# Kernel tuning notes

Measured on AMD Instinct MI355X. Metric: run time of the kernel, lower is better.

Reference implementation:

```python
import math
import jax, jax.numpy as jnp
import numpy as np

B, SX, SY, D, H = 2, 1024, 1024, 1024, 16
FULL = 1536   # padded (full_q == full_k) frame length for the two-source attention
N_CTX = 2048  # causal bias buffer size
HD = D // H
LENS_X = np.array([1024, 700])
LENS_Y = np.array([1024, 850])


def _heads(t):
    b, s, d = t.shape
    return t.reshape(b, s, H, HD).transpose(0, 2, 1, 3)  # [B,H,S,HD]


def _merge(t):
    b, h, s, hd = t.shape
    return t.transpose(0, 2, 1, 3).reshape(b, s, h * hd)


def setup_inputs() -> dict:
    key = jax.random.key(0)
    ks = jax.random.split(key, 8)
    s = 0.02
    # ragged pack/unpack index lists: take = positions in the FULL frame, fill = positions in the shrunk frame
    x_take_b = np.concatenate([np.full(l, b, np.int32) for b, l in enumerate(LENS_X)])
    x_take_p = np.concatenate([(FULL - l + np.arange(l)).astype(np.int32) for l in LENS_X])  # right-aligned
    x_fill_b = x_take_b.copy()
    x_fill_p = np.concatenate([np.arange(l, dtype=np.int32) for l in LENS_X])
    y_take_b = np.concatenate([np.full(l, b, np.int32) for b, l in enumerate(LENS_Y)])
    y_take_p = np.concatenate([np.arange(l, dtype=np.int32) for l in LENS_Y])  # left-aligned
    y_fill_b = y_take_b.copy()
    y_fill_p = y_take_p.copy()
    # additive padding mask for the self-attention over shrunk x
    mask = np.full((B, 1, 1, SX), -10000.0, np.float32)
    for b, l in enumerate(LENS_X):
        mask[b, :, :, :l] = 0.0
    return {
        "x": jax.random.normal(ks[0], (B, SX, D), jnp.float32),
        "y": jax.random.normal(ks[1], (B, SY, D), jnp.float32),
        "attention_mask_x": jnp.asarray(mask),
        "W_attn": jax.random.normal(ks[2], (D, 3 * D), jnp.float32) * s,
        "b_attn": jnp.zeros((3 * D,), jnp.float32),
        "W_2a": jax.random.normal(ks[3], (D, D), jnp.float32) * s,
        "b_2a": jnp.zeros((D,), jnp.float32),
        "W_2b": jax.random.normal(ks[4], (D, 2 * D), jnp.float32) * s,
        "b_2b": jnp.zeros((2 * D,), jnp.float32),
        "W_proj": jax.random.normal(ks[5], (2 * D, D), jnp.float32) * s,
        "b_proj": jnp.zeros((D,), jnp.float32),
        "x_take_b": jnp.asarray(x_take_b), "x_take_p": jnp.asarray(x_take_p),
        "x_fill_b": jnp.asarray(x_fill_b), "x_fill_p": jnp.asarray(x_fill_p),
        "y_take_b": jnp.asarray(y_take_b), "y_take_p": jnp.asarray(y_take_p),
        "y_fill_b": jnp.asarray(y_fill_b), "y_fill_p": jnp.asarray(y_fill_p),
    }


def reference(x, y, attention_mask_x, W_attn, b_attn, W_2a, b_2a, W_2b, b_2b,
              W_proj, b_proj, x_take_b, x_take_p, x_fill_b, x_fill_p,
              y_take_b, y_take_p, y_fill_b, y_fill_p):
    causal = jnp.tril(jnp.ones((N_CTX, N_CTX), jnp.float32))
    inv_sqrt = 1.0 / math.sqrt(HD)

    # --- branch 1: causal self-attention on shrunk x ---
    qkv = x @ W_attn + b_attn
    q, k, v = jnp.split(qkv, 3, axis=2)
    q, k, v = _heads(q), _heads(k), _heads(v)
    w = jnp.einsum('bhqd,bhkd->bhqk', q, k) * inv_sqrt  # [B,H,SX,SX]
    b1 = causal[:SX, :SX]
    w = w * b1 - 10000.0 * (1.0 - b1) + attention_mask_x
    a = jnp.einsum('bhqk,bhkd->bhqd', jax.nn.softmax(w, axis=-1), v)
    a = _merge(a)  # [B,SX,D]

    # --- branch 2: two-source attention with ragged expand/shrink ---
    q2 = _heads(x @ W_2a + b_2a)                      # [B,H,SX,HD]
    k2, v2 = jnp.split(y @ W_2b + b_2b, 2, axis=2)
    k2, v2 = _heads(k2), _heads(v2)                   # [B,H,SY,HD]
    w2 = jnp.einsum('bhqd,bhkd->bhqk', q2, k2)        # [B,H,SX,SY] (unscaled yet)
    # expand key dim: shrunk SY -> FULL
    temp = jnp.zeros((B, H, SX, FULL), w2.dtype)
    temp = temp.at[y_take_b, :, :, y_take_p].set(w2[y_fill_b, :, :, y_fill_p])
    # expand query dim: shrunk SX -> FULL
    new_w = jnp.zeros((B, H, FULL, FULL), w2.dtype)
    new_w = new_w.at[x_take_b, :, x_take_p, :].set(temp[x_fill_b, :, x_fill_p, :])
    new_v = jnp.zeros((B, H, FULL, HD), v2.dtype)
    new_v = new_v.at[y_take_b, :, y_take_p, :].set(v2[y_fill_b, :, y_fill_p, :])
    kmask = jnp.full((B, 1, 1, FULL), -10000.0, w2.dtype)
    kmask = kmask.at[y_take_b, :, :, y_take_p].set(0.0)
    new_w = new_w * inv_sqrt
    b2 = causal[:FULL, :FULL]  # ns-nd == 0 since full_q == full_k
    new_w = new_w * b2 - 10000.0 * (1.0 - b2) + kmask
    a2 = jnp.einsum('bhqk,bhkd->bhqd', jax.nn.softmax(new_w, axis=-1), new_v)  # [B,H,FULL,HD]
    # shrink query dim back: FULL -> SX
    a2s = jnp.zeros((B, H, SX, HD), a2.dtype)
    a2s = a2s.at[x_fill_b, :, x_fill_p, :].set(a2[x_take_b, :, x_take_p, :])
    a2m = _merge(a2s)  # [B,SX,D]

    out = jnp.concatenate([a, a2m], axis=2) @ W_proj + b_proj  # [B,SX,D]
    return out
```

## Files before the change

kernel.cpp:

```cpp
#include <hip/hip_runtime.h>
#include <hip/hip_bf16.h>

typedef __bf16 bf16;
typedef __attribute__((ext_vector_type(4))) __bf16 bf16x4;
typedef __attribute__((ext_vector_type(8))) __bf16 bf16x8;
typedef __attribute__((ext_vector_type(4))) float floatx4;

__device__ __forceinline__ void gl_lds16(const bf16* g, bf16* l) {
  __builtin_amdgcn_global_load_lds(
      (const __attribute__((address_space(1))) void*)g,
      (__attribute__((address_space(3))) void*)l, 16, 0, 0);
}

__global__ __launch_bounds__(256) void sentinel_kernel(float* out, int n, float code) {
  int i = blockIdx.x * 256 + threadIdx.x;
  if (i < n) out[i] = code;
}

struct TP { const float* W; bf16* WT; int K; int N; int bxn; int bid0; };

__global__ __launch_bounds__(256) void prep_kernel(TP t0, TP t1, TP t2, TP t3,
                                                   const float* __restrict__ x,
                                                   const float* __restrict__ y,
                                                   bf16* __restrict__ xb,
                                                   bf16* __restrict__ yb) {
  __shared__ bf16 tile[32][33];
  int bid = blockIdx.x;
  if (bid < 8192) {
    TP t = t0;
    if (bid >= t3.bid0) t = t3;
    else if (bid >= t2.bid0) t = t2;
    else if (bid >= t1.bid0) t = t1;
    int rb = bid - t.bid0;
    int bx = rb % t.bxn, by = rb / t.bxn;
    int n0 = bx * 32, k0 = by * 32;
    int tx = threadIdx.x & 31, ty = threadIdx.x >> 5;
#pragma unroll
    for (int i = 0; i < 32; i += 8)
      tile[ty + i][tx] = (bf16)t.W[(size_t)(k0 + ty + i) * t.N + n0 + tx];
    __syncthreads();
#pragma unroll
    for (int i = 0; i < 32; i += 8)
      t.WT[(size_t)(n0 + ty + i) * t.K + k0 + tx] = tile[tx][ty + i];
  } else {
    long base = (long)(bid - 8192) * 4096 + (long)threadIdx.x * 16;
    const float* src = x; bf16* dst = xb; long idx = base;
    if (base >= 2097152) { src = y; dst = yb; idx = base - 2097152; }
    floatx4 v0 = *(const floatx4*)(src + idx);
    floatx4 v1 = *(const floatx4*)(src + idx + 4);
    floatx4 v2 = *(const floatx4*)(src + idx + 8);
    floatx4 v3 = *(const floatx4*)(src + idx + 12);
    bf16x8 o0, o1;
#pragma unroll
    for (int i = 0; i < 4; ++i) {
      o0[i] = (bf16)v0[i]; o0[4 + i] = (bf16)v1[i];
      o1[i] = (bf16)v2[i]; o1[4 + i] = (bf16)v3[i];
    }
    *(bf16x8*)(dst + idx) = o0;
    *(bf16x8*)(dst + idx + 8) = o1;
  }
}

struct GP { const bf16* A; const bf16* WT; const float* bias; bf16* C; bf16* VT;
            int N; int ldc; int vcol0; int bxn; int bid0; };

__global__ __launch_bounds__(256) void proj3_kernel(GP g0, GP g1, GP g2) {
  __shared__ __attribute__((aligned(16))) bf16 As[128 * 32];
  __shared__ __attribute__((aligned(16))) bf16 Bs[128 * 32];
  int bid = blockIdx.x;
  GP g = g0;
  if (bid >= g2.bid0) g = g2;
  else if (bid >= g1.bid0) g = g1;
  int rb = bid - g.bid0;
  int row0 = (rb / g.bxn) * 128, col0 = (rb % g.bxn) * 128;
  const int K = 1024;
  int tid = threadIdx.x;
  int lane = tid & 63, wave = tid >> 6;
  int quad = lane >> 4, l16 = lane & 15;
  int wm = wave >> 1, wn = wave & 1;
  floatx4 acc[4][4] = {};
  for (int k0 = 0; k0 < K; k0 += 32) {
#pragma unroll
    for (int s = 0; s < 2; ++s) {
      int chunk = s * 256 + tid;
      int r = chunk >> 2, c = (chunk & 3) * 8;
      gl_lds16(g.WT + (size_t)(col0 + r) * K + k0 + c, Bs + (size_t)chunk * 8);
      gl_lds16(g.A + (size_t)(row0 + r) * K + k0 + c, As + (size_t)chunk * 8);
    }
    __syncthreads();
    bf16x8 afr[4], bfr[4];
#pragma unroll
    for (int r = 0; r < 4; ++r)
      afr[r] = *(const bf16x8*)(As + (wm * 64 + r * 16 + l16) * 32 + quad * 8);
#pragma unroll
    for (int c = 0; c < 4; ++c)
      bfr[c] = *(const bf16x8*)(Bs + (wn * 64 + c * 16 + l16) * 32 + quad * 8);
#pragma unroll
    for (int r = 0; r < 4; ++r)
#pragma unroll
      for (int c = 0; c < 4; ++c)
        acc[r][c] = __builtin_amdgcn_mfma_f32_16x16x32_bf16(afr[r], bfr[c], acc[r][c], 0, 0, 0);
    __syncthreads();
  }
  int inV = (col0 >= g.vcol0);
#pragma unroll
  for (int c = 0; c < 4; ++c) {
    int gcol = col0 + wn * 64 + c * 16 + l16;
    float bv = g.bias[gcol];
    if (inV) {
      int vcol = gcol - g.vcol0;
      int hh = vcol >> 6, dd = vcol & 63;
#pragma unroll
      for (int r = 0; r < 4; ++r) {
        int row = row0 + wm * 64 + r * 16 + quad * 4;
        int bb = row >> 10, key = row & 1023;
        bf16x4 pk;
#pragma unroll
        for (int e = 0; e < 4; ++e) pk[e] = (bf16)(acc[r][c][e] + bv);
        *(bf16x4*)(g.VT + ((size_t)((bb << 4) + hh)) * 65536 + (size_t)dd * 1024 + key) = pk;
      }
    } else {
#pragma unroll
      for (int r = 0; r < 4; ++r) {
        int grow = row0 + wm * 64 + r * 16 + quad * 4;
#pragma unroll
        for (int e = 0; e < 4; ++e)
          g.C[(size_t)(grow + e) * g.ldc + gcol] = (bf16)(acc[r][c][e] + bv);
      }
    }
  }
}

__global__ __launch_bounds__(256) void gemm_out_kernel(const bf16* __restrict__ A,
                                                       const bf16* __restrict__ WT,
                                                       const float* __restrict__ bias,
                                                       float* __restrict__ C,
                                                       int N, int K) {
  __shared__ __attribute__((aligned(16))) bf16 As[64 * 32];
  __shared__ __attribute__((aligned(16))) bf16 Bs[64 * 32];
  int tid = threadIdx.x;
  int lane = tid & 63, wave = tid >> 6;
  int quad = lane >> 4, l16 = lane & 15;
  int row0 = blockIdx.y * 64, col0 = blockIdx.x * 64;
  floatx4 acc[4] = {};
  for (int k0 = 0; k0 < K; k0 += 32) {
    int r = tid >> 2, c = (tid & 3) * 8;
    gl_lds16(A + (size_t)(row0 + r) * K + k0 + c, As + (size_t)tid * 8);
    gl_lds16(WT + (size_t)(col0 + r) * K + k0 + c, Bs + (size_t)tid * 8);
    __syncthreads();
    bf16x8 af = *(const bf16x8*)(As + (wave * 16 + l16) * 32 + quad * 8);
#pragma unroll
    for (int nt = 0; nt < 4; ++nt) {
      bf16x8 bf = *(const bf16x8*)(Bs + (nt * 16 + l16) * 32 + quad * 8);
      acc[nt] = __builtin_amdgcn_mfma_f32_16x16x32_bf16(af, bf, acc[nt], 0, 0, 0);
    }
    __syncthreads();
  }
#pragma unroll
  for (int nt = 0; nt < 4; ++nt) {
    int gcol = col0 + nt * 16 + l16;
    float bv = bias[gcol];
#pragma unroll
    for (int e = 0; e < 4; ++e) {
      int grow = row0 + wave * 16 + quad * 4 + e;
      C[(size_t)grow * N + gcol] = acc[nt][e] + bv;
    }
  }
}

struct AP {
  const bf16* Q; const bf16* K; const bf16* VT; bf16* O;
  int qstride, kstride, ostride;
  long qbatch, kbatch, obatch;
  int coff0, coff1, klen0, klen1, qv0, qv1;
};

__global__ __launch_bounds__(512) void attn2x_kernel(AP a0, AP a1, float scale) {
  __shared__ __attribute__((aligned(16))) bf16 Ks[2][64 * 64];
  __shared__ __attribute__((aligned(16))) bf16 Vs[2][64 * 64];
  __shared__ __attribute__((aligned(16))) bf16 Ps[8][16 * 72];
  AP a = (blockIdx.x >> 8) ? a1 : a0;
  int tid = threadIdx.x;
  int lane = tid & 63, w = tid >> 6;
  int quad = lane >> 4, l16 = lane & 15;
  int r = blockIdx.x & 255;
  int b = r >> 7, h = (r >> 3) & 15, qt = r & 7;
  int coff = b ? a.coff1 : a.coff0;
  int klen = b ? a.klen1 : a.klen0;
  int qv = b ? a.qv1 : a.qv0;
  int qbase = qt * 128;
  int wq0 = qbase + w * 16;
  int qi = wq0 + l16;
  const bf16* Q   = a.Q + (size_t)b * a.qbatch + h * 64;
  const bf16* Kp  = a.K + (size_t)b * a.kbatch + h * 64;
  const bf16* VTp = a.VT + (size_t)(b * 16 + h) * 65536;
  bf16* O = a.O + (size_t)b * a.obatch + h * 64;

  bf16x8 aq0 = *(const bf16x8*)(Q + (size_t)qi * a.qstride + quad * 8);
  bf16x8 aq1 = *(const bf16x8*)(Q + (size_t)qi * a.qstride + 32 + quad * 8);

  floatx4 o[4] = {};
  float part = 0.f;

  int kend = klen < qbase + 128 + coff ? klen : qbase + 128 + coff;
  int nblk = (kend + 63) >> 6;
  int wkend0 = wq0 + 16 + coff;
  int wkend = klen < wkend0 ? klen : wkend0;

  const float KSC = scale * 1.44269504f;
  const float KOFF = -5.77078016f;

  auto stage = [&](int buf, int j0) {
    int row = tid >> 3, ch = tid & 7;
    gl_lds16(Kp + (size_t)(j0 + row) * a.kstride + ((ch ^ (row & 7)) * 8),
             Ks[buf] + (size_t)tid * 8);
    gl_lds16(VTp + (size_t)row * 1024 + j0 + ((ch ^ (row & 7)) * 8),
             Vs[buf] + (size_t)tid * 8);
  };

  stage(0, 0);
  for (int t = 0; t < nblk; ++t) {
    int j0 = t * 64;
    __syncthreads();
    if (t + 1 < nblk) stage((t + 1) & 1, j0 + 64);
    if (j0 >= wkend) continue;
    const bf16* Kt = Ks[t & 1];
    const bf16* Vt = Vs[t & 1];

    floatx4 sv[4];
#pragma unroll
    for (int nt = 0; nt < 4; ++nt) {
      int key = nt * 16 + l16;
      int sl0 = key * 8 + (quad ^ (key & 7));
      int sl1 = key * 8 + ((quad + 4) ^ (key & 7));
      bf16x8 bk0 = *(const bf16x8*)(Kt + (size_t)sl0 * 8);
      bf16x8 bk1 = *(const bf16x8*)(Kt + (size_t)sl1 * 8);
      floatx4 z = {};
      z = __builtin_amdgcn_mfma_f32_16x16x32_bf16(bk0, aq0, z, 0, 0, 0);
      z = __builtin_amdgcn_mfma_f32_16x16x32_bf16(bk1, aq1, z, 0, 0, 0);
      sv[nt] = z;
    }
    bool fullv = (j0 + 63 <= wq0 + coff) && (j0 + 63 < klen);
#pragma unroll
    for (int nt = 0; nt < 4; ++nt) {
      bf16x4 pk;
#pragma unroll
      for (int e = 0; e < 4; ++e) {
        float arg = fmaf(sv[nt][e], KSC, KOFF);
        if (!fullv) {
          int j = j0 + nt * 16 + quad * 4 + e;
          arg = (j <= qi + coff && j < klen) ? arg : -60.0f;
        }
        float p = exp2f(arg);
        part += p;
        pk[e] = (bf16)p;
      }
      *(bf16x4*)(Ps[w] + l16 * 72 + nt * 16 + quad * 4) = pk;
    }
    bf16x8 pb0 = *(const bf16x8*)(Ps[w] + l16 * 72 + quad * 8);
    bf16x8 pb1 = *(const bf16x8*)(Ps[w] + l16 * 72 + 32 + quad * 8);
#pragma unroll
    for (int ct = 0; ct < 4; ++ct) {
      int dd = ct * 16 + l16;
      int sl0 = dd * 8 + (quad ^ (dd & 7));
      int sl1 = dd * 8 + ((quad + 4) ^ (dd & 7));
      bf16x8 va0 = *(const bf16x8*)(Vt + (size_t)sl0 * 8);
      bf16x8 va1 = *(const bf16x8*)(Vt + (size_t)sl1 * 8);
      o[ct] = __builtin_amdgcn_mfma_f32_16x16x32_bf16(va0, pb0, o[ct], 0, 0, 0);
      o[ct] = __builtin_amdgcn_mfma_f32_16x16x32_bf16(va1, pb1, o[ct], 0, 0, 0);
    }
  }
  part += __shfl_xor(part, 16);
  part += __shfl_xor(part, 32);
  float rinv = 1.0f / part;
#pragma unroll
  for (int ct = 0; ct < 4; ++ct) {
    bf16x4 pk;
#pragma unroll
    for (int e = 0; e < 4; ++e) {
      float val = o[ct][e] * rinv;
      if (qi >= qv) val = 0.f;
      pk[e] = (bf16)val;
    }
    *(bf16x4*)(O + (size_t)qi * a.ostride + ct * 16 + quad * 4) = pk;
  }
}

extern "C" void kernel_launch(void* const* d_in, const int* in_sizes, int n_in,
                              void* d_out, int out_size, void* d_ws, size_t ws_size,
                              hipStream_t stream) {
  const float* x      = (const float*)d_in[0];
  const float* y      = (const float*)d_in[1];
  const float* W_attn = (const float*)d_in[3];
  const float* b_attn = (const float*)d_in[4];
  const float* W_2a   = (const float*)d_in[5];
  const float* b_2a   = (const float*)d_in[6];
  const float* W_2b   = (const float*)d_in[7];
  const float* b_2b   = (const float*)d_in[8];
  const float* W_proj = (const float*)d_in[9];
  const float* b_proj = (const float*)d_in[10];
  bf16* ws = (bf16*)d_ws;
  float* out = (float*)d_out;

  const int LX0 = 1024, LX1 = 700, LY0 = 1024, LY1 = 850;
  const float scale = 0.125f;
  const size_t WS_FAST = (size_t)25165824 * 2;

  if (ws_size < WS_FAST) {
    sentinel_kernel<<<(out_size + 255) / 256, 256, 0, stream>>>(
        out, out_size, (float)(ws_size >> 20) + 10.0f);
    return;
  }

  bf16* qk1  = ws;
  bf16* q2   = ws + (size_t) 4194304;
  bf16* k2   = ws + (size_t) 6291456;
  bf16* VT1  = ws + (size_t) 8388608;
  bf16* VT2  = ws + (size_t)10485760;
  bf16* xb   = ws + (size_t)12582912;
  bf16* yb   = ws + (size_t)14680064;
  bf16* cat  = ws + (size_t)12582912;
  bf16* WaT  = ws + (size_t)16777216;
  bf16* W2aT = ws + (size_t)19922944;
  bf16* W2bT = ws + (size_t)20971520;
  bf16* WpT  = ws + (size_t)23068672;

  TP t0 = {W_attn, WaT, 1024, 3072, 96, 0};
  TP t1 = {W_2a, W2aT, 1024, 1024, 32, 3072};
  TP t2 = {W_2b, W2bT, 1024, 2048, 64, 4096};
  TP t3 = {W_proj, WpT, 2048, 1024, 32, 6144};
  prep_kernel<<<9216, 256, 0, stream>>>(t0, t1, t2, t3, x, y, xb, yb);

  GP g0 = {xb, WaT, b_attn, qk1, VT1, 3072, 2048, 2048, 24, 0};
  GP g1 = {xb, W2aT, b_2a, q2, nullptr, 1024, 1024, 1 << 30, 8, 384};
  GP g2 = {yb, W2bT, b_2b, k2, VT2, 2048, 1024, 1024, 16, 512};
  proj3_kernel<<<768, 256, 0, stream>>>(g0, g1, g2);

  AP a0 = {qk1, qk1 + 1024, VT1, cat, 2048, 2048, 2048,
           (long)1024 * 2048, (long)1024 * 2048, (long)1024 * 2048,
           0, 0, LX0, LX1, 1024, 1024};
  AP a1 = {q2, k2, VT2, cat + 1024, 1024, 1024, 2048,
           (long)1024 * 1024, (long)1024 * 1024, (long)1024 * 2048,
           1536 - LX0, 1536 - LX1, LY0, LY1, LX0, LX1};
  attn2x_kernel<<<512, 512, 0, stream>>>(a0, a1, scale);

  gemm_out_kernel<<<dim3(16, 32), 256, 0, stream>>>(cat, WpT, b_proj, out, 1024, 2048);
}
```

Baseline: 236.5 us.

## Widen GEMM K-tiles to 64 with XOR-swizzled LDS and vectorize weight transpose

The weight-transpose prep now uses 64x64 fp32 tiles with float4 loads and bf16x4 stores, so it needs fewer blocks and fewer, wider memory transactions. Both the QKV projection GEMM and the output GEMM move from a K step of 32 to 64. Their LDS tiles are XOR-swizzled on 16-byte chunks to avoid bank conflicts, which halves the number of barriers per K sweep. The cost is twice the LDS per block, which may lower occupancy.

```diff
diff --git a/kernel.cpp b/kernel.cpp
--- a/kernel.cpp
+++ b/kernel.cpp
@@ -24,26 +24,34 @@
                                                    const float* __restrict__ y,
                                                    bf16* __restrict__ xb,
                                                    bf16* __restrict__ yb) {
-  __shared__ bf16 tile[32][33];
   int bid = blockIdx.x;
-  if (bid < 8192) {
+  int tid = threadIdx.x;
+  if (bid < 2048) {
+    __shared__ float tile[64][65];
     TP t = t0;
     if (bid >= t3.bid0) t = t3;
     else if (bid >= t2.bid0) t = t2;
     else if (bid >= t1.bid0) t = t1;
     int rb = bid - t.bid0;
-    int bx = rb % t.bxn, by = rb / t.bxn;
-    int n0 = bx * 32, k0 = by * 32;
-    int tx = threadIdx.x & 31, ty = threadIdx.x >> 5;
-#pragma unroll
-    for (int i = 0; i < 32; i += 8)
-      tile[ty + i][tx] = (bf16)t.W[(size_t)(k0 + ty + i) * t.N + n0 + tx];
-    __syncthreads();
-#pragma unroll
-    for (int i = 0; i < 32; i += 8)
-      t.WT[(size_t)(n0 + ty + i) * t.K + k0 + tx] = tile[tx][ty + i];
+    int n0 = (rb % t.bxn) * 64, k0 = (rb / t.bxn) * 64;
+    int tx = tid & 15, ty = tid >> 4;
+#pragma unroll
+    for (int i = 0; i < 4; ++i) {
+      floatx4 v = *(const floatx4*)(t.W + (size_t)(k0 + ty + 16 * i) * t.N + n0 + tx * 4);
+#pragma unroll
+      for (int j = 0; j < 4; ++j) tile[ty + 16 * i][tx * 4 + j] = v[j];
+    }
+    __syncthreads();
+#pragma unroll
+    for (int i = 0; i < 4; ++i) {
+      int nr = ty + 16 * i;
+      bf16x4 o;
+#pragma unroll
+      for (int j = 0; j < 4; ++j) o[j] = (bf16)tile[tx * 4 + j][nr];
+      *(bf16x4*)(t.WT + (size_t)(n0 + nr) * t.K + k0 + tx * 4) = o;
+    }
   } else {
-    long base = (long)(bid - 8192) * 4096 + (long)threadIdx.x * 16;
+    long base = (long)(bid - 2048) * 4096 + (long)tid * 16;
     const float* src = x; bf16* dst = xb; long idx = base;
     if (base >= 2097152) { src = y; dst = yb; idx = base - 2097152; }
     floatx4 v0 = *(const floatx4*)(src + idx);
@@ -65,8 +73,8 @@
             int N; int ldc; int vcol0; int bxn; int bid0; };
 
 __global__ __launch_bounds__(256) void proj3_kernel(GP g0, GP g1, GP g2) {
-  __shared__ __attribute__((aligned(16))) bf16 As[128 * 32];
-  __shared__ __attribute__((aligned(16))) bf16 Bs[128 * 32];
+  __shared__ __attribute__((aligned(16))) bf16 As[128 * 64];
+  __shared__ __attribute__((aligned(16))) bf16 Bs[128 * 64];
   int bid = blockIdx.x;
   GP g = g0;
   if (bid >= g2.bid0) g = g2;
@@ -79,27 +87,36 @@
   int quad = lane >> 4, l16 = lane & 15;
   int wm = wave >> 1, wn = wave & 1;
   floatx4 acc[4][4] = {};
-  for (int k0 = 0; k0 < K; k0 += 32) {
-#pragma unroll
-    for (int s = 0; s < 2; ++s) {
-      int chunk = s * 256 + tid;
-      int r = chunk >> 2, c = (chunk & 3) * 8;
-      gl_lds16(g.WT + (size_t)(col0 + r) * K + k0 + c, Bs + (size_t)chunk * 8);
-      gl_lds16(g.A + (size_t)(row0 + r) * K + k0 + c, As + (size_t)chunk * 8);
-    }
-    __syncthreads();
-    bf16x8 afr[4], bfr[4];
-#pragma unroll
-    for (int r = 0; r < 4; ++r)
-      afr[r] = *(const bf16x8*)(As + (wm * 64 + r * 16 + l16) * 32 + quad * 8);
-#pragma unroll
-    for (int c = 0; c < 4; ++c)
-      bfr[c] = *(const bf16x8*)(Bs + (wn * 64 + c * 16 + l16) * 32 + quad * 8);
-#pragma unroll
-    for (int r = 0; r < 4; ++r)
-#pragma unroll
-      for (int c = 0; c < 4; ++c)
-        acc[r][c] = __builtin_amdgcn_mfma_f32_16x16x32_bf16(afr[r], bfr[c], acc[r][c], 0, 0, 0);
+  for (int k0 = 0; k0 < K; k0 += 64) {
+#pragma unroll
+    for (int s = 0; s < 4; ++s) {
+      int sl = s * 256 + tid;
+      int r = sl >> 3, o = sl & 7;
+      int c = (o ^ (r & 7)) * 8;
+      gl_lds16(g.WT + (size_t)(col0 + r) * K + k0 + c, Bs + (size_t)sl * 8);
+      gl_lds16(g.A + (size_t)(row0 + r) * K + k0 + c, As + (size_t)sl * 8);
+    }
+    __syncthreads();
+#pragma unroll
+    for (int kk = 0; kk < 2; ++kk) {
+      int ko = kk * 4 + quad;
+      bf16x8 afr[4], bfr[4];
+#pragma unroll
+      for (int r = 0; r < 4; ++r) {
+        int m = wm * 64 + r * 16 + l16;
+        afr[r] = *(const bf16x8*)(As + (size_t)(m * 8 + (ko ^ (m & 7))) * 8);
+      }
+#pragma unroll
+      for (int c = 0; c < 4; ++c) {
+        int n = wn * 64 + c * 16 + l16;
+        bfr[c] = *(const bf16x8*)(Bs + (size_t)(n * 8 + (ko ^ (n & 7))) * 8);
+      }
+#pragma unroll
+      for (int r = 0; r < 4; ++r)
+#pragma unroll
+        for (int c = 0; c < 4; ++c)
+          acc[r][c] = __builtin_amdgcn_mfma_f32_16x16x32_bf16(afr[r], bfr[c], acc[r][c], 0, 0, 0);
+    }
     __syncthreads();
   }
   int inV = (col0 >= g.vcol0);
@@ -136,23 +153,34 @@
                                                        const float* __restrict__ bias,
                                                        float* __restrict__ C,
                                                        int N, int K) {
-  __shared__ __attribute__((aligned(16))) bf16 As[64 * 32];
-  __shared__ __attribute__((aligned(16))) bf16 Bs[64 * 32];
+  __shared__ __attribute__((aligned(16))) bf16 As[64 * 64];
+  __shared__ __attribute__((aligned(16))) bf16 Bs[64 * 64];
   int tid = threadIdx.x;
   int lane = tid & 63, wave = tid >> 6;
   int quad = lane >> 4, l16 = lane & 15;
   int row0 = blockIdx.y * 64, col0 = blockIdx.x * 64;
   floatx4 acc[4] = {};
-  for (int k0 = 0; k0 < K; k0 += 32) {
-    int r = tid >> 2, c = (tid & 3) * 8;
-    gl_lds16(A + (size_t)(row0 + r) * K + k0 + c, As + (size_t)tid * 8);
-    gl_lds16(WT + (size_t)(col0 + r) * K + k0 + c, Bs + (size_t)tid * 8);
-    __syncthreads();
-    bf16x8 af = *(const bf16x8*)(As + (wave * 16 + l16) * 32 + quad * 8);
-#pragma unroll
-    for (int nt = 0; nt < 4; ++nt) {
-      bf16x8 bf = *(const bf16x8*)(Bs + (nt * 16 + l16) * 32 + quad * 8);
-      acc[nt] = __builtin_amdgcn_mfma_f32_16x16x32_bf16(af, bf, acc[nt], 0, 0, 0);
+  for (int k0 = 0; k0 < K; k0 += 64) {
+#pragma unroll
+    for (int s = 0; s < 2; ++s) {
+      int sl = s * 256 + tid;
+      int r = sl >> 3, o = sl & 7;
+      int c = (o ^ (r & 7)) * 8;
+      gl_lds16(A + (size_t)(row0 + r) * K + k0 + c, As + (size_t)sl * 8);
+      gl_lds16(WT + (size_t)(col0 + r) * K + k0 + c, Bs + (size_t)sl * 8);
+    }
+    __syncthreads();
+#pragma unroll
+    for (int kk = 0; kk < 2; ++kk) {
+      int ko = kk * 4 + quad;
+      int m = wave * 16 + l16;
+      bf16x8 af = *(const bf16x8*)(As + (size_t)(m * 8 + (ko ^ (m & 7))) * 8);
+#pragma unroll
+      for (int nt = 0; nt < 4; ++nt) {
+        int n = nt * 16 + l16;
+        bf16x8 bf = *(const bf16x8*)(Bs + (size_t)(n * 8 + (ko ^ (n & 7))) * 8);
+        acc[nt] = __builtin_amdgcn_mfma_f32_16x16x32_bf16(af, bf, acc[nt], 0, 0, 0);
+      }
     }
     __syncthreads();
   }
@@ -325,11 +353,11 @@
   bf16* W2bT = ws + (size_t)20971520;
   bf16* WpT  = ws + (size_t)23068672;
 
-  TP t0 = {W_attn, WaT, 1024, 3072, 96, 0};
-  TP t1 = {W_2a, W2aT, 1024, 1024, 32, 3072};
-  TP t2 = {W_2b, W2bT, 1024, 2048, 64, 4096};
-  TP t3 = {W_proj, WpT, 2048, 1024, 32, 6144};
-  prep_kernel<<<9216, 256, 0, stream>>>(t0, t1, t2, t3, x, y, xb, yb);
+  TP t0 = {W_attn, WaT, 1024, 3072, 48, 0};
+  TP t1 = {W_2a, W2aT, 1024, 1024, 16, 768};
+  TP t2 = {W_2b, W2bT, 1024, 2048, 32, 1024};
+  TP t3 = {W_proj, WpT, 2048, 1024, 16, 1536};
+  prep_kernel<<<3072, 256, 0, stream>>>(t0, t1, t2, t3, x, y, xb, yb);
 
   GP g0 = {xb, WaT, b_attn, qk1, VT1, 3072, 2048, 2048, 24, 0};
   GP g1 = {xb, W2aT, b_2a, q2, nullptr, 1024, 1024, 1 << 30, 8, 384};
```

Result: no change. 232.7 us (-1.6%).
